# Optimization experiments

Hardware: AMD Instinct MI355X
Metric: run time of the kernel (lower is better)

The kernel has to match this reference:

```python
import jax, jax.numpy as jnp
import numpy as np

H, KB = 8, 8          # z_num grid (h, k)
OB, IB = 64, 64       # per-call weight block [OB, IB, K]
K, L = 9, 9           # kernel dims of exe_unet_weight and unet_1d_weights
ZD, PD, DH = 64, 16, 128  # z_dim, pde_inputs dim, hypernet hidden


def setup_inputs() -> dict:
    key = jax.random.key(0)
    k1, k2, k3, k4, k5 = jax.random.split(key, 5)
    # z params: torch.fmod(randn, 2) as in the original __init__
    z_all = jnp.fmod(jax.random.normal(k1, (H * KB, ZD), jnp.float32), 2.0)
    W1 = jax.random.normal(k2, (DH, ZD + PD), jnp.float32) * 0.1
    b1 = jnp.zeros((DH,), jnp.float32)
    W2 = jax.random.normal(k3, (OB * IB * K, DH), jnp.float32) * 0.02
    b2 = jnp.zeros((OB * IB * K,), jnp.float32)
    unet_1d_weights = jax.random.normal(k4, (H * OB, KB * IB, L), jnp.float32)
    pde_inputs = jax.random.normal(k5, (PD,), jnp.float32)
    return {"z_all": z_all, "W1": W1, "b1": b1, "W2": W2, "b2": b2,
            "unet_1d_weights": unet_1d_weights, "pde_inputs": pde_inputs}


def reference(z_all, W1, b1, W2, b2, unet_1d_weights, pde_inputs):
    # Batched hypernet: one GEMM over all h*k z vectors instead of h*k calls.
    x = jnp.concatenate([z_all, jnp.broadcast_to(pde_inputs, (H * KB, PD))], axis=1)  # [hk, ZD+PD]
    hid = jax.nn.relu(x @ W1.T + b1)                    # [hk, DH]
    w = (hid @ W2.T + b2).reshape(H, KB, OB, IB, K)      # per-cell blocks
    # cat(dim=1) within row, cat(dim=0) across rows -> [H*OB, KB*IB, K]
    exe_unet_weight = w.transpose(0, 2, 1, 3, 4).reshape(H * OB, KB * IB, K)
    # broadcast outer product over kernel dims
    w_2d = jnp.einsum('oik,oil->oikl', exe_unet_weight, unet_1d_weights)
    return w_2d
```

## Files before the change

### kernel.cpp

```cpp
#include <hip/hip_runtime.h>

#define ZD_ 64
#define PD_ 16
#define DH_ 128
#define LDS_STRIDE 132

__global__ void hid_kernel(const float* __restrict__ z_all,
                           const float* __restrict__ W1,
                           const float* __restrict__ b1,
                           const float* __restrict__ pde,
                           float* __restrict__ hid) {
    int gid = blockIdx.x * 256 + threadIdx.x;
    int r = gid >> 7;
    int d = gid & 127;
    const float* w = W1 + d * (ZD_ + PD_);
    const float* z = z_all + r * ZD_;
    float acc = b1[d];
    #pragma unroll 8
    for (int c = 0; c < ZD_; ++c) acc += z[c] * w[c];
    #pragma unroll
    for (int c = 0; c < PD_; ++c) acc += pde[c] * w[ZD_ + c];
    hid[gid] = fmaxf(acc, 0.0f);
}

__global__ __launch_bounds__(256) void exe_kernel(
        const float* __restrict__ hid,
        const float* __restrict__ W2,
        const float* __restrict__ b2,
        float* __restrict__ exe) {
    __shared__ __align__(16) float s_tile[64 * LDS_STRIDE];
    int tid = threadIdx.x;
    int n0  = blockIdx.x * 64;

    const float4* g4 = reinterpret_cast<const float4*>(W2 + (size_t)n0 * DH_);
    #pragma unroll
    for (int j = 0; j < 8; ++j) {
        int g  = j * 256 + tid;
        int nl = g >> 5;
        int k0 = (g & 31) * 4;
        *reinterpret_cast<float4*>(&s_tile[nl * LDS_STRIDE + k0]) = g4[g];
    }
    __syncthreads();

    int wave   = __builtin_amdgcn_readfirstlane(tid >> 6);
    int lane   = tid & 63;
    int hkbase = wave * 16;
    const float* hbase = hid + (size_t)hkbase * DH_;

    float bias = b2[n0 + lane];
    float acc[16];
    #pragma unroll
    for (int j = 0; j < 16; ++j) acc[j] = bias;

    const float* trow = s_tile + lane * LDS_STRIDE;
    #pragma unroll 4
    for (int c = 0; c < 32; ++c) {
        int k0 = c * 4;
        float4 v = *reinterpret_cast<const float4*>(trow + k0);
        #pragma unroll
        for (int j = 0; j < 16; ++j) {
            float4 hv = *reinterpret_cast<const float4*>(hbase + j * DH_ + k0);
            acc[j] += hv.x * v.x + hv.y * v.y + hv.z * v.z + hv.w * v.w;
        }
    }

    int ob = n0 / 576;
    int r  = n0 % 576 + lane;
    #pragma unroll
    for (int j = 0; j < 16; ++j) {
        int hk = hkbase + j;
        int h = hk >> 3, kb = hk & 7;
        exe[(size_t)(h * 64 + ob) * 4608 + kb * 576 + r] = acc[j];
    }
}

__global__ void outer_kernel(const float* __restrict__ exe,
                             const float* __restrict__ unet,
                             float* __restrict__ out) {
    __shared__ float s_e[576], s_u[576];
    int b = blockIdx.x;
    int o = b >> 3, c = b & 7;
    size_t base9 = (size_t)o * 4608 + (size_t)c * 576;
    const float4* e4 = reinterpret_cast<const float4*>(exe + base9);
    const float4* u4 = reinterpret_cast<const float4*>(unet + base9);
    int tid = threadIdx.x;
    if (tid < 144) {
        reinterpret_cast<float4*>(s_e)[tid] = e4[tid];
        reinterpret_cast<float4*>(s_u)[tid] = u4[tid];
    }
    __syncthreads();
    float4* o4 = reinterpret_cast<float4*>(out + (size_t)o * 41472 + (size_t)c * 5184);
    for (int idx = tid; idx < 1296; idx += 256) {
        int e0 = idx * 4;
        float4 v;
        float* vp = &v.x;
        #pragma unroll
        for (int j = 0; j < 4; ++j) {
            int e = e0 + j;
            int p = e / 81;
            int rem = e - p * 81;
            int k = rem / 9;
            int l = rem - k * 9;
            vp[j] = s_e[p * 9 + k] * s_u[p * 9 + l];
        }
        o4[idx] = v;
    }
}

extern "C" void kernel_launch(void* const* d_in, const int* in_sizes, int n_in,
                              void* d_out, int out_size, void* d_ws, size_t ws_size,
                              hipStream_t stream) {
    const float* z_all = (const float*)d_in[0];
    const float* W1    = (const float*)d_in[1];
    const float* b1    = (const float*)d_in[2];
    const float* W2    = (const float*)d_in[3];
    const float* b2    = (const float*)d_in[4];
    const float* unet  = (const float*)d_in[5];
    const float* pde   = (const float*)d_in[6];
    float* out = (float*)d_out;

    float* ws  = (float*)d_ws;
    float* hid = ws;
    float* exe = ws + 8192;

    hid_kernel<<<32, 256, 0, stream>>>(z_all, W1, b1, pde, hid);
    exe_kernel<<<576, 256, 0, stream>>>(hid, W2, b2, exe);
    outer_kernel<<<4096, 256, 0, stream>>>(exe, unet, out);
}
```

Baseline: 156.2 us.

## Fuse hypernet GEMM with outer-product expansion into one kernel

Merges the exe GEMM kernel and the outer-product kernel into a single kernel. Each block computes 36 output columns (4 input channels × 9 taps) for all 64 hk cells and keeps the resulting weights in LDS. It then writes the expanded 9×9 outputs directly. This removes the exe intermediate round trip through global memory and one launch. In exchange, each block now reads hid from global/L2 per thread, redistributes the GEMM work, and makes strided unet loads.

```diff
diff --git a/kernel.cpp b/kernel.cpp
--- a/kernel.cpp
+++ b/kernel.cpp
@@ -3,7 +3,6 @@
 #define ZD_ 64
 #define PD_ 16
 #define DH_ 128
-#define LDS_STRIDE 132
 
 __global__ void hid_kernel(const float* __restrict__ z_all,
                            const float* __restrict__ W1,
@@ -23,87 +22,78 @@
     hid[gid] = fmaxf(acc, 0.0f);
 }
 
-__global__ __launch_bounds__(256) void exe_kernel(
+__global__ __launch_bounds__(256, 4) void fused_kernel(
         const float* __restrict__ hid,
         const float* __restrict__ W2,
         const float* __restrict__ b2,
-        float* __restrict__ exe) {
-    __shared__ __align__(16) float s_tile[64 * LDS_STRIDE];
+        const float* __restrict__ unet,
+        float* __restrict__ out) {
+    __shared__ __align__(16) float s_w2[36 * 132];
+    __shared__ float s_exe[64 * 36];
+    __shared__ float s_un [64 * 36];
+
     int tid = threadIdx.x;
-    int n0  = blockIdx.x * 64;
+    int b   = blockIdx.x;
+    int ob  = b >> 4;
+    int ibg = b & 15;
+    int n0  = ob * 576 + ibg * 36;
 
     const float4* g4 = reinterpret_cast<const float4*>(W2 + (size_t)n0 * DH_);
-    #pragma unroll
-    for (int j = 0; j < 8; ++j) {
-        int g  = j * 256 + tid;
-        int nl = g >> 5;
-        int k0 = (g & 31) * 4;
-        *reinterpret_cast<float4*>(&s_tile[nl * LDS_STRIDE + k0]) = g4[g];
+    for (int j = tid; j < 1152; j += 256) {
+        int row  = j >> 5;
+        int col4 = j & 31;
+        *reinterpret_cast<float4*>(&s_w2[row * 132 + col4 * 4]) = g4[j];
+    }
+
+    for (int idx = tid; idx < 2304; idx += 256) {
+        int rr = idx / 36;
+        int jj = idx - rr * 36;
+        int h  = rr >> 3, kb = rr & 7;
+        size_t ub = ((size_t)((h * 64 + ob) * 512 + kb * 64 + ibg * 4)) * 9;
+        s_un[idx] = unet[ub + jj];
     }
     __syncthreads();
 
-    int wave   = __builtin_amdgcn_readfirstlane(tid >> 6);
-    int lane   = tid & 63;
-    int hkbase = wave * 16;
-    const float* hbase = hid + (size_t)hkbase * DH_;
+    int cell = tid >> 2;
+    int ib   = tid & 3;
+    const float4* h4p = reinterpret_cast<const float4*>(hid + cell * DH_);
+    const float*  wb  = s_w2 + ib * 9 * 132;
+    const float*  bp  = b2 + n0 + ib * 9;
 
-    float bias = b2[n0 + lane];
-    float acc[16];
+    float acc[9];
     #pragma unroll
-    for (int j = 0; j < 16; ++j) acc[j] = bias;
+    for (int k = 0; k < 9; ++k) acc[k] = bp[k];
 
-    const float* trow = s_tile + lane * LDS_STRIDE;
     #pragma unroll 4
     for (int c = 0; c < 32; ++c) {
-        int k0 = c * 4;
-        float4 v = *reinterpret_cast<const float4*>(trow + k0);
+        float4 h4 = h4p[c];
         #pragma unroll
-        for (int j = 0; j < 16; ++j) {
-            float4 hv = *reinterpret_cast<const float4*>(hbase + j * DH_ + k0);
-            acc[j] += hv.x * v.x + hv.y * v.y + hv.z * v.z + hv.w * v.w;
+        for (int k = 0; k < 9; ++k) {
+            float4 w4 = *reinterpret_cast<const float4*>(wb + k * 132 + c * 4);
+            acc[k] += h4.x * w4.x + h4.y * w4.y + h4.z * w4.z + h4.w * w4.w;
         }
     }
+    #pragma unroll
+    for (int k = 0; k < 9; ++k) s_exe[tid * 9 + k] = acc[k];
+    __syncthreads();
 
-    int ob = n0 / 576;
-    int r  = n0 % 576 + lane;
-    #pragma unroll
-    for (int j = 0; j < 16; ++j) {
-        int hk = hkbase + j;
-        int h = hk >> 3, kb = hk & 7;
-        exe[(size_t)(h * 64 + ob) * 4608 + kb * 576 + r] = acc[j];
-    }
-}
-
-__global__ void outer_kernel(const float* __restrict__ exe,
-                             const float* __restrict__ unet,
-                             float* __restrict__ out) {
-    __shared__ float s_e[576], s_u[576];
-    int b = blockIdx.x;
-    int o = b >> 3, c = b & 7;
-    size_t base9 = (size_t)o * 4608 + (size_t)c * 576;
-    const float4* e4 = reinterpret_cast<const float4*>(exe + base9);
-    const float4* u4 = reinterpret_cast<const float4*>(unet + base9);
-    int tid = threadIdx.x;
-    if (tid < 144) {
-        reinterpret_cast<float4*>(s_e)[tid] = e4[tid];
-        reinterpret_cast<float4*>(s_u)[tid] = u4[tid];
-    }
-    __syncthreads();
-    float4* o4 = reinterpret_cast<float4*>(out + (size_t)o * 41472 + (size_t)c * 5184);
-    for (int idx = tid; idx < 1296; idx += 256) {
-        int e0 = idx * 4;
+    for (int idx = tid; idx < 5184; idx += 256) {
+        int rr = idx / 81;
+        int q  = idx - rr * 81;
         float4 v;
         float* vp = &v.x;
         #pragma unroll
-        for (int j = 0; j < 4; ++j) {
-            int e = e0 + j;
-            int p = e / 81;
-            int rem = e - p * 81;
-            int k = rem / 9;
-            int l = rem - k * 9;
-            vp[j] = s_e[p * 9 + k] * s_u[p * 9 + l];
+        for (int j2 = 0; j2 < 4; ++j2) {
+            int e   = q * 4 + j2;
+            int ibb = e / 81;
+            int rem = e - ibb * 81;
+            int k   = rem / 9;
+            int l   = rem - k * 9;
+            vp[j2] = s_exe[rr * 36 + ibb * 9 + k] * s_un[rr * 36 + ibb * 9 + l];
         }
-        o4[idx] = v;
+        int h = rr >> 3, kb = rr & 7;
+        size_t base = ((size_t)((h * 64 + ob) * 512 + kb * 64 + ibg * 4)) * 81;
+        reinterpret_cast<float4*>(out + base)[q] = v;
     }
 }
 
@@ -119,11 +109,8 @@
     const float* pde   = (const float*)d_in[6];
     float* out = (float*)d_out;
 
-    float* ws  = (float*)d_ws;
-    float* hid = ws;
-    float* exe = ws + 8192;
+    float* hid = (float*)d_ws;
 
     hid_kernel<<<32, 256, 0, stream>>>(z_all, W1, b1, pde, hid);
-    exe_kernel<<<576, 256, 0, stream>>>(hid, W2, b2, exe);
-    outer_kernel<<<4096, 256, 0, stream>>>(exe, unet, out);
+    fused_kernel<<<1024, 256, 0, stream>>>(hid, W2, b2, unet, out);
 }
```

Result: faster. 143.1 us (-8.4%).
